# Kernel optimization log

Measured on AMD Instinct MI355X. Metric: run time of the kernel, lower is better.

The kernel has to match this reference:

```python
import jax, jax.numpy as jnp
import numpy as np

N, E, G, ND, H, C, L = 100000, 640000, 1000, 128, 128, 10, 4
ATOMS_PER_GRAPH = 100  # N = G * ATOMS_PER_GRAPH
NEG_SLOPE = 0.01  # nn.LeakyReLU default


def setup_inputs() -> dict:
    key = jax.random.key(0)
    ks = jax.random.split(key, 16)
    s = 0.05
    return {
        "node_attr": jax.random.normal(ks[0], (N, ND), jnp.float32),
        "edge_index": jax.random.randint(ks[1], (2, E), 0, N, jnp.int64),
        "num_atoms": jnp.full((G,), ATOMS_PER_GRAPH, dtype=jnp.int64),
        "enc_W": jax.random.normal(ks[2], (ND, H), jnp.float32) * s,
        "enc_b": jnp.zeros((H,), jnp.float32),
        "gcn_W": jax.random.normal(ks[3], (L, H, H), jnp.float32) * s,
        "gcn_b": jnp.zeros((L, H), jnp.float32),
        "r_W1": jax.random.normal(ks[4], (H, H), jnp.float32) * s,
        "r_b1": jnp.zeros((H,), jnp.float32),
        "r_W2": jax.random.normal(ks[5], (H, H), jnp.float32) * s,
        "r_b2": jnp.zeros((H,), jnp.float32),
        "s_W1": jax.random.normal(ks[6], (H, H), jnp.float32) * s,
        "s_b1": jnp.zeros((H,), jnp.float32),
        "s_W2": jax.random.normal(ks[7], (H, H), jnp.float32) * s,
        "s_b2": jnp.zeros((H,), jnp.float32),
        "fin_W": jax.random.normal(ks[8], (H, C), jnp.float32) * s,
        "fin_b": jnp.zeros((C,), jnp.float32),
    }


def _leaky(x):
    return jnp.where(x > 0, x, NEG_SLOPE * x)


def reference(node_attr, edge_index, num_atoms, enc_W, enc_b, gcn_W, gcn_b,
              r_W1, r_b1, r_W2, r_b2, s_W1, s_b1, s_W2, s_b2, fin_W, fin_b):
    dst, src = edge_index[0], edge_index[1]
    # degree normalization constant across layers: deg(i) = in-edge count, divide by deg+1
    deg = jax.ops.segment_sum(jnp.ones((E,), node_attr.dtype), dst, num_segments=N)
    inv_deg = 1.0 / (deg + 1.0)  # [N]

    x = node_attr @ enc_W + enc_b  # [N, H]
    for l in range(L):
        h = x @ gcn_W[l] + gcn_b[l]
        agg = jax.ops.segment_sum(h[src], dst, num_segments=N)  # scatter_sum over dst
        x = (h + agg) * inv_deg[:, None]

    # GateMLP: ReLuMLP(x) * SigmoidMLP(x)
    r = _leaky(_leaky(x @ r_W1 + r_b1) @ r_W2 + r_b2)
    g = jax.nn.sigmoid(_leaky(x @ s_W1 + s_b1) @ s_W2 + s_b2)
    x = r * g  # [N, H]

    # graph pooling: scatter_mean over graph ids
    graph_mask = jnp.repeat(jnp.arange(G), num_atoms, total_repeat_length=N)
    gsum = jax.ops.segment_sum(x, graph_mask, num_segments=G)
    cnt = jax.ops.segment_sum(jnp.ones((N,), x.dtype), graph_mask, num_segments=G)
    graph_attr = gsum / jnp.maximum(cnt, 1.0)[:, None]  # [G, H]
    return graph_attr @ fin_W + fin_b  # [G, C]
```

## Files before the change

kernel.cpp:

```cpp
#include <hip/hip_runtime.h>
#include <hip/hip_bf16.h>
#include <cstddef>
#include <cstdint>

#define CAP 32
#define LEAK 0.01f

typedef __attribute__((ext_vector_type(8))) short short8v;
typedef __attribute__((ext_vector_type(4))) float float4v;

__device__ __forceinline__ unsigned short f2bf(float f) {
    uint32_t u = __float_as_uint(f);
    uint32_t r = (u + 0x7FFFu + ((u >> 16) & 1u)) >> 16;
    return (unsigned short)r;
}
__device__ __forceinline__ float bf2f(unsigned short s) {
    return __uint_as_float(((uint32_t)s) << 16);
}

__device__ __forceinline__ void load_wf(const unsigned short* __restrict__ Wpack,
                                        int w, int fr, int fg, short8v wf[2][4]) {
    const short8v* Wp = (const short8v*)Wpack;
#pragma unroll
    for (int t = 0; t < 2; ++t)
#pragma unroll
        for (int kc = 0; kc < 4; ++kc)
            wf[t][kc] = Wp[(kc * 4 + fg) * 128 + w * 32 + t * 16 + fr];
}

__device__ __forceinline__ void load_wf_f32(const float* __restrict__ W,
                                            int w, int fr, int fg, short8v wf[2][4]) {
#pragma unroll
    for (int t = 0; t < 2; ++t) {
        const int n = w * 32 + t * 16 + fr;
#pragma unroll
        for (int kc = 0; kc < 4; ++kc) {
            short8v v;
#pragma unroll
            for (int j = 0; j < 8; ++j)
                v[j] = (short)f2bf(W[(size_t)(kc * 32 + fg * 8 + j) * 128 + n]);
            wf[t][kc] = v;
        }
    }
}

__device__ __forceinline__ void mfma_tile(const unsigned short* As, int fr, int fg,
                                          const short8v wf[2][4], float4v acc[4][2]) {
#pragma unroll
    for (int m = 0; m < 4; ++m) {
        acc[m][0] = (float4v){0.f, 0.f, 0.f, 0.f};
        acc[m][1] = (float4v){0.f, 0.f, 0.f, 0.f};
    }
#pragma unroll
    for (int kc = 0; kc < 4; ++kc) {
        short8v a[4];
#pragma unroll
        for (int m = 0; m < 4; ++m) {
            int row = m * 16 + fr;
            int cb = (kc * 64 + fg * 16) ^ ((row & 7) << 4);
            a[m] = *(const short8v*)((const char*)As + row * 256 + cb);
        }
#pragma unroll
        for (int m = 0; m < 4; ++m) {
            acc[m][0] = __builtin_amdgcn_mfma_f32_16x16x32_bf16(a[m], wf[0][kc], acc[m][0], 0, 0, 0);
            acc[m][1] = __builtin_amdgcn_mfma_f32_16x16x32_bf16(a[m], wf[1][kc], acc[m][1], 0, 0, 0);
        }
    }
}

__global__ __launch_bounds__(256) void prep(const int* __restrict__ ei, int E_,
                                            int* __restrict__ cnt,
                                            int* __restrict__ bucket,
                                            const float* __restrict__ node_attr,
                                            unsigned short* __restrict__ bx, int Nn,
                                            const float* __restrict__ enc_W,
                                            const float* __restrict__ gcn_W,
                                            const float* __restrict__ rw1,
                                            const float* __restrict__ rw2,
                                            const float* __restrict__ sw1,
                                            const float* __restrict__ sw2,
                                            const float* __restrict__ enc_b,
                                            const float* __restrict__ gcn_b,
                                            const float* __restrict__ rb1,
                                            const float* __restrict__ sb1,
                                            unsigned short* __restrict__ wpack,
                                            unsigned short* __restrict__ foldbuf,
                                            float* __restrict__ fbias,
                                            const int* __restrict__ na,
                                            int* __restrict__ goff, int G_,
                                            int NB_EDGE, int NB_CVT) {
    const int b = blockIdx.x;
    const int tid = threadIdx.x;

    if (b < NB_EDGE) {
        int e = (b * 256 + tid) * 4;
        if (e >= E_) return;
        if (e + 4 <= E_) {
            int4 d4 = *(const int4*)&ei[e];
            int4 s4 = *(const int4*)&ei[(size_t)E_ + e];
            int p0 = atomicAdd(&cnt[d4.x], 1);
            int p1 = atomicAdd(&cnt[d4.y], 1);
            int p2 = atomicAdd(&cnt[d4.z], 1);
            int p3 = atomicAdd(&cnt[d4.w], 1);
            if (p0 < CAP) bucket[(size_t)d4.x * CAP + p0] = s4.x;
            if (p1 < CAP) bucket[(size_t)d4.y * CAP + p1] = s4.y;
            if (p2 < CAP) bucket[(size_t)d4.z * CAP + p2] = s4.z;
            if (p3 < CAP) bucket[(size_t)d4.w * CAP + p3] = s4.w;
        } else {
            for (; e < E_; ++e) {
                int d = ei[e], s = ei[(size_t)E_ + e];
                int p = atomicAdd(&cnt[d], 1);
                if (p < CAP) bucket[(size_t)d * CAP + p] = s;
            }
        }
        return;
    }
    if (b < NB_EDGE + NB_CVT) {
        size_t i8 = ((size_t)(b - NB_EDGE) * 256 + tid) * 8;
        if (i8 < (size_t)Nn * 128) {
            const float* ap = node_attr + i8;
            float4v p = *(const float4v*)ap;
            float4v q = *(const float4v*)(ap + 4);
            short8v v;
            v[0] = (short)f2bf(p[0]); v[1] = (short)f2bf(p[1]);
            v[2] = (short)f2bf(p[2]); v[3] = (short)f2bf(p[3]);
            v[4] = (short)f2bf(q[0]); v[5] = (short)f2bf(q[1]);
            v[6] = (short)f2bf(q[2]); v[7] = (short)f2bf(q[3]);
            *(short8v*)(bx + i8) = v;
        }
        return;
    }
    if (b < NB_EDGE + NB_CVT + 72) {
        int pb = b - (NB_EDGE + NB_CVT);
        int m = pb >> 3;
        if (m != 6 && m != 8) return;
        int idx = (pb & 7) * 256 + tid;
        const float* W = (m == 6) ? rw2 : sw2;
        int n = idx & 127;
        int fg = (idx >> 7) & 3;
        int kc = idx >> 9;
        short8v v;
#pragma unroll
        for (int j = 0; j < 8; ++j)
            v[j] = (short)f2bf(W[(size_t)(kc * 32 + fg * 8 + j) * 128 + n]);
        *(short8v*)(wpack + (size_t)m * 16384 + (size_t)idx * 8) = v;
        return;
    }
    int fb = b - (NB_EDGE + NB_CVT + 72);
    if (fb == 0) {
        __shared__ unsigned short As[64 * 128];
        __shared__ float betaL[128];

        if (tid < 128) betaL[tid] = enc_b[tid];
        __syncthreads();
        for (int l = 0; l < 4; ++l) {
            const float* Wl = gcn_W + (size_t)l * 16384;
            float acc = 0.f;
            if (tid < 128) {
                acc = gcn_b[l * 128 + tid];
                for (int k = 0; k < 128; ++k)
                    acc = fmaf(betaL[k], Wl[(size_t)k * 128 + tid], acc);
            }
            __syncthreads();
            if (tid < 128) betaL[tid] = acc;
            __syncthreads();
        }
        if (tid < 128) {
            float a1 = rb1[tid], a2 = sb1[tid];
            for (int k = 0; k < 128; ++k) {
                float bk = betaL[k];
                a1 = fmaf(bk, rw1[(size_t)k * 128 + tid], a1);
                a2 = fmaf(bk, sw1[(size_t)k * 128 + tid], a2);
            }
            fbias[128 + tid] = a1;
            fbias[256 + tid] = a2;
        }
        __syncthreads();

        const int lane = tid & 63;
        const int w = tid >> 6;
        const int fr = lane & 15;
        const int fg = lane >> 4;
        unsigned short* f0 = foldbuf;
        unsigned short* f1 = foldbuf + 32768;
        const float* Ls[5] = {gcn_W + (size_t)3 * 16384, gcn_W + (size_t)2 * 16384,
                              gcn_W + (size_t)1 * 16384, gcn_W, enc_W};

        for (int p = 0; p < 5; ++p) {
            const unsigned short* inb = (p == 0) ? nullptr : (((p - 1) & 1) == 0 ? f0 : f1);
            unsigned short* outb = (p == 4) ? (wpack + (size_t)9 * 16384)
                                            : ((p & 1) == 0 ? f0 : f1);
            const float* Lp = Ls[p];
#pragma unroll 1
            for (int rt = 0; rt < 2; ++rt) {
                {
                    const int r = tid >> 2;
                    const int cg = tid & 3;
                    const float* Ap = Lp + (size_t)(rt * 64 + r) * 128 + cg * 32;
                    char* lbase = (char*)As + r * 256;
#pragma unroll
                    for (int i = 0; i < 4; ++i) {
                        float4v pv = *(const float4v*)(Ap + i * 8);
                        float4v qv = *(const float4v*)(Ap + i * 8 + 4);
                        short8v v;
                        v[0] = (short)f2bf(pv[0]); v[1] = (short)f2bf(pv[1]);
                        v[2] = (short)f2bf(pv[2]); v[3] = (short)f2bf(pv[3]);
                        v[4] = (short)f2bf(qv[0]); v[5] = (short)f2bf(qv[1]);
                        v[6] = (short)f2bf(qv[2]); v[7] = (short)f2bf(qv[3]);
                        int cb = (cg * 64 + i * 16) ^ ((r & 7) << 4);
                        *(short8v*)(lbase + cb) = v;
                    }
                }
                __syncthreads();

#pragma unroll 1
                for (int panel = 0; panel < 2; ++panel) {
                    short8v wf[2][4];
                    if (p == 0) load_wf_f32(panel ? sw1 : rw1, w, fr, fg, wf);
                    else        load_wf(inb + panel * 16384, w, fr, fg, wf);
                    float4v acc[4][2];
                    mfma_tile(As, fr, fg, wf, acc);
                    unsigned short* dstp = outb + panel * 16384;
#pragma unroll
                    for (int t = 0; t < 2; ++t)
#pragma unroll
                        for (int m = 0; m < 4; ++m)
#pragma unroll
                            for (int q = 0; q < 4; ++q) {
                                int r = rt * 64 + m * 16 + fg * 4 + q;
                                int c = w * 32 + t * 16 + fr;
                                dstp[(size_t)((((r >> 5) * 4 + ((r >> 3) & 3)) * 128 + c) * 8)
                                     + (r & 7)] = f2bf(acc[m][t][q]);
                            }
                }
                __syncthreads();
            }
            __threadfence();
            __syncthreads();
        }
        return;
    }
    if (fb == 1) {
        __shared__ int sh[256];
        int base = tid * 4;
        int v0 = (base + 0 < G_) ? na[base + 0] : 0;
        int v1 = (base + 1 < G_) ? na[base + 1] : 0;
        int v2 = (base + 2 < G_) ? na[base + 2] : 0;
        int v3 = (base + 3 < G_) ? na[base + 3] : 0;
        int s = v0 + v1 + v2 + v3;
        sh[tid] = s;
        __syncthreads();
        for (int ofs = 1; ofs < 256; ofs <<= 1) {
            int u = (tid >= ofs) ? sh[tid - ofs] : 0;
            __syncthreads();
            sh[tid] += u;
            __syncthreads();
        }
        int run = sh[tid] - s;
        if (tid == 0) goff[0] = 0;
        run += v0; if (base + 0 < G_) goff[base + 1] = run;
        run += v1; if (base + 1 < G_) goff[base + 2] = run;
        run += v2; if (base + 2 < G_) goff[base + 3] = run;
        run += v3; if (base + 3 < G_) goff[base + 4] = run;
    }
}

__device__ __forceinline__ void acc8(float a[8], uint4 v, float m) {
    a[0] = fmaf(m, bf2f((unsigned short)(v.x & 0xffff)), a[0]);
    a[1] = fmaf(m, bf2f((unsigned short)(v.x >> 16)), a[1]);
    a[2] = fmaf(m, bf2f((unsigned short)(v.y & 0xffff)), a[2]);
    a[3] = fmaf(m, bf2f((unsigned short)(v.y >> 16)), a[3]);
    a[4] = fmaf(m, bf2f((unsigned short)(v.z & 0xffff)), a[4]);
    a[5] = fmaf(m, bf2f((unsigned short)(v.z >> 16)), a[5]);
    a[6] = fmaf(m, bf2f((unsigned short)(v.w & 0xffff)), a[6]);
    a[7] = fmaf(m, bf2f((unsigned short)(v.w >> 16)), a[7]);
}

__device__ __forceinline__ void issue4(const char* __restrict__ xb, int2 prep_,
                                       int gl, int l16, int Nn, int jb, uint4 V[4]) {
    const int sl = gl + (jb >> 1);
    int s0 = __shfl(prep_.x, sl);
    int s1 = __shfl(prep_.y, sl);
    int s2 = __shfl(prep_.x, sl + 1);
    int s3 = __shfl(prep_.y, sl + 1);
    s0 = min(max(s0, 0), Nn - 1);
    s1 = min(max(s1, 0), Nn - 1);
    s2 = min(max(s2, 0), Nn - 1);
    s3 = min(max(s3, 0), Nn - 1);
    V[0] = *(const uint4*)(xb + (size_t)s0 * 256 + l16 * 16);
    V[1] = *(const uint4*)(xb + (size_t)s1 * 256 + l16 * 16);
    V[2] = *(const uint4*)(xb + (size_t)s2 * 256 + l16 * 16);
    V[3] = *(const uint4*)(xb + (size_t)s3 * 256 + l16 * 16);
}

__device__ __forceinline__ void consume4(float a[8], const uint4 V[4], int jb, int d) {
    acc8(a, V[0], (jb + 0 < d) ? 1.f : 0.f);
    acc8(a, V[1], (jb + 1 < d) ? 1.f : 0.f);
    acc8(a, V[2], (jb + 2 < d) ? 1.f : 0.f);
    acc8(a, V[3], (jb + 3 < d) ? 1.f : 0.f);
}

__global__ __launch_bounds__(256, 4) void agg_pass(const unsigned short* __restrict__ x,
                                                   const int* __restrict__ bucket,
                                                   const int* __restrict__ cnt,
                                                   unsigned short* __restrict__ xout,
                                                   int Nn) {
    const int tid = threadIdx.x;
    const int lane = tid & 63;
    const int w = tid >> 6;
    const int row0 = blockIdx.x * 64;
    const int l16 = lane & 15;
    const int g = lane >> 4;
    const int gl = lane & 48;
    const char* xb = (const char*)x;

    int cfull = 0;
    if (lane < 16) {
        int gn = row0 + w * 16 + lane;
        if (gn >= Nn) gn = Nn - 1;
        cfull = cnt[gn];
    }
    uint4 own[4];
    int2 pre[4];
#pragma unroll
    for (int p = 0; p < 4; ++p) {
        int gn = row0 + w * 16 + p * 4 + g;
        if (gn >= Nn) gn = Nn - 1;
        own[p] = *(const uint4*)(xb + (size_t)gn * 256 + l16 * 16);
        pre[p] = *(const int2*)&bucket[(size_t)gn * CAP + 2 * l16];
    }

#pragma unroll
    for (int p = 0; p < 4; ++p) {
        const int n = p * 4 + g;
        const int r = w * 16 + n;
        const int dfull = __shfl(cfull, n);
        const float id = 1.0f / (float)(dfull + 1);
        const int d = min(dfull, CAP);

        uint4 VA[4], VB[4];
        issue4(xb, pre[p], gl, l16, Nn, 0, VA);

        float a[8];
        {
            uint4 o = own[p];
            a[0] = bf2f((unsigned short)(o.x & 0xffff));
            a[1] = bf2f((unsigned short)(o.x >> 16));
            a[2] = bf2f((unsigned short)(o.y & 0xffff));
            a[3] = bf2f((unsigned short)(o.y >> 16));
            a[4] = bf2f((unsigned short)(o.z & 0xffff));
            a[5] = bf2f((unsigned short)(o.z >> 16));
            a[6] = bf2f((unsigned short)(o.w & 0xffff));
            a[7] = bf2f((unsigned short)(o.w >> 16));
        }

        int j = 0;
        while (true) {
            if (j + 4 < d) issue4(xb, pre[p], gl, l16, Nn, j + 4, VB);
            consume4(a, VA, j, d);
            j += 4;
            if (j >= d) break;
            if (j + 4 < d) issue4(xb, pre[p], gl, l16, Nn, j + 4, VA);
            consume4(a, VB, j, d);
            j += 4;
            if (j >= d) break;
        }

#pragma unroll
        for (int i = 0; i < 8; ++i) a[i] *= id;
        uint4 o;
        o.x = (uint32_t)f2bf(a[0]) | ((uint32_t)f2bf(a[1]) << 16);
        o.y = (uint32_t)f2bf(a[2]) | ((uint32_t)f2bf(a[3]) << 16);
        o.z = (uint32_t)f2bf(a[4]) | ((uint32_t)f2bf(a[5]) << 16);
        o.w = (uint32_t)f2bf(a[6]) | ((uint32_t)f2bf(a[7]) << 16);
        int node = row0 + r;
        if (node < Nn)
            *(uint4*)((char*)xout + (size_t)node * 256 + l16 * 16) = o;
    }
}

__global__ __launch_bounds__(512, 4) void gate_fused(const unsigned short* __restrict__ x,
                                                     const unsigned short* __restrict__ wpack,
                                                     const float* __restrict__ rb1f,
                                                     const float* __restrict__ rb2,
                                                     const float* __restrict__ sb1f,
                                                     const float* __restrict__ sb2,
                                                     unsigned short* __restrict__ out, int M) {
    __shared__ unsigned short Ws[2 * 128 * 128];
    const int tid = threadIdx.x;
    const int lane = tid & 63;
    const int w = tid >> 6;
    const int l16 = lane & 15;
    const int fg = lane >> 4;
    const int row0 = blockIdx.x * 128 + w * 16;

    int xr = row0 + l16;
    if (xr >= M) xr = M - 1;
    short8v xbf[4];
#pragma unroll
    for (int kc = 0; kc < 4; ++kc)
        xbf[kc] = *(const short8v*)(x + (size_t)xr * 128 + kc * 32 + fg * 8);

    const short8v* WL = (const short8v*)Ws;
    uint32_t upR[8][2], upS[8][2];

    union { uint32_t u[4]; short8v v; } cvt;

#define STAGE2(mi0, mi1)                                                      \
    {                                                                         \
        const short8v* s0 = (const short8v*)(wpack + (size_t)(mi0) * 16384);  \
        const short8v* s1 = (const short8v*)(wpack + (size_t)(mi1) * 16384);  \
        short8v* dst = (short8v*)Ws;                                          \
        _Pragma("unroll") for (int i = 0; i < 4; ++i)                         \
            dst[i * 512 + tid] = s0[i * 512 + tid];                          \
        _Pragma("unroll") for (int i = 0; i < 4; ++i)                         \
            dst[2048 + i * 512 + tid] = s1[i * 512 + tid];                    \
    }

#define PASS1(OFS, BIAS, UP)                                                  \
    _Pragma("unroll") for (int nt = 0; nt < 8; ++nt) {                        \
        float4v acc = (float4v){0.f, 0.f, 0.f, 0.f};                          \
        _Pragma("unroll") for (int kc = 0; kc < 4; ++kc)                      \
            acc = __builtin_amdgcn_mfma_f32_16x16x32_bf16(                    \
                WL[(OFS) + (kc * 4 + fg) * 128 + nt * 16 + l16], xbf[kc], acc, 0, 0, 0); \
        _Pragma("unroll") for (int q = 0; q < 4; ++q) {                       \
            float v = acc[q] + (BIAS)[nt * 16 + fg * 4 + q];                  \
            acc[q] = v > 0.f ? v : LEAK * v;                                  \
        }                                                                     \
        UP[nt][0] = (uint32_t)f2bf(acc[0]) | ((uint32_t)f2bf(acc[1]) << 16);  \
        UP[nt][1] = (uint32_t)f2bf(acc[2]) | ((uint32_t)f2bf(acc[3]) << 16);  \
    }

#define MKUF(UP, UF)                                                          \
    _Pragma("unroll") for (int kc = 0; kc < 4; ++kc) {                        \
        uint32_t pr0, pr1, pr2, pr3;                                          \
        {                                                                     \
            int srcl = (((2 * fg + 0) & 3) << 4) + l16;                       \
            uint32_t lo = __shfl((int)UP[2 * kc][0], srcl);                   \
            uint32_t hi = __shfl((int)UP[2 * kc + 1][0], srcl);               \
            pr0 = (fg & 2) ? hi : lo;                                         \
            lo = __shfl((int)UP[2 * kc][1], srcl);                            \
            hi = __shfl((int)UP[2 * kc + 1][1], srcl);                        \
            pr1 = (fg & 2) ? hi : lo;                                         \
        }                                                                     \
        {                                                                     \
            int srcl = (((2 * fg + 1) & 3) << 4) + l16;                       \
            uint32_t lo = __shfl((int)UP[2 * kc][0], srcl);                   \
            uint32_t hi = __shfl((int)UP[2 * kc + 1][0], srcl);               \
            pr2 = (fg & 2) ? hi : lo;                                         \
            lo = __shfl((int)UP[2 * kc][1], srcl);                            \
            hi = __shfl((int)UP[2 * kc + 1][1], srcl);                        \
            pr3 = (fg & 2) ? hi : lo;                                         \
        }                                                                     \
        cvt.u[0] = pr0; cvt.u[1] = pr1; cvt.u[2] = pr2; cvt.u[3] = pr3;       \
        UF[kc] = cvt.v;                                                       \
    }

    STAGE2(9, 10);
    __syncthreads();
    PASS1(0, rb1f, upR);
    PASS1(2048, sb1f, upS);
    __syncthreads();

    STAGE2(6, 8);
    __syncthreads();

    short8v uf[4];
    MKUF(upR, uf);
    float4v rf[8];
#pragma unroll
    for (int t2 = 0; t2 < 8; ++t2) {
        float4v acc = (float4v){0.f, 0.f, 0.f, 0.f};
#pragma unroll
        for (int kc = 0; kc < 4; ++kc)
            acc = __builtin_amdgcn_mfma_f32_16x16x32_bf16(
                uf[kc], WL[(kc * 4 + fg) * 128 + t2 * 16 + l16], acc, 0, 0, 0);
        const float bv = rb2[t2 * 16 + l16];
#pragma unroll
        for (int q = 0; q < 4; ++q) {
            float v = acc[q] + bv;
            rf[t2][q] = v > 0.f ? v : LEAK * v;
        }
    }

    MKUF(upS, uf);
#pragma unroll
    for (int t2 = 0; t2 < 8; ++t2) {
        float4v acc = (float4v){0.f, 0.f, 0.f, 0.f};
#pragma unroll
        for (int kc = 0; kc < 4; ++kc)
            acc = __builtin_amdgcn_mfma_f32_16x16x32_bf16(
                uf[kc], WL[2048 + (kc * 4 + fg) * 128 + t2 * 16 + l16], acc, 0, 0, 0);
        const float bv = sb2[t2 * 16 + l16];
#pragma unroll
        for (int q = 0; q < 4; ++q) {
            int row = row0 + fg * 4 + q;
            if (row < M) {
                float gg = 1.f / (1.f + __expf(-(acc[q] + bv)));
                out[(size_t)row * 128 + t2 * 16 + l16] = f2bf(gg * rf[t2][q]);
            }
        }
    }
#undef STAGE2
#undef PASS1
#undef MKUF
}

__global__ void pool(const unsigned short* __restrict__ x, const int* __restrict__ goff,
                     float* __restrict__ gattr, int G_) {
    int g = blockIdx.x * 2 + (threadIdx.x >> 7);
    if (g >= G_) return;
    int d = threadIdx.x & 127;
    int a0 = goff[g], a1 = goff[g + 1];
    float s0 = 0.f, s1 = 0.f, s2 = 0.f, s3 = 0.f;
    int a = a0;
    for (; a + 4 <= a1; a += 4) {
        s0 += bf2f(__builtin_nontemporal_load(&x[(size_t)(a + 0) * 128 + d]));
        s1 += bf2f(__builtin_nontemporal_load(&x[(size_t)(a + 1) * 128 + d]));
        s2 += bf2f(__builtin_nontemporal_load(&x[(size_t)(a + 2) * 128 + d]));
        s3 += bf2f(__builtin_nontemporal_load(&x[(size_t)(a + 3) * 128 + d]));
    }
    for (; a < a1; ++a) s0 += bf2f(__builtin_nontemporal_load(&x[(size_t)a * 128 + d]));
    float s = (s0 + s1) + (s2 + s3);
    float c = (float)max(a1 - a0, 1);
    gattr[(size_t)g * 128 + d] = s / c;
}

__global__ void final_gemm(const float* __restrict__ gattr, const float* __restrict__ fW,
                           const float* __restrict__ fb, float* __restrict__ out,
                           int G_, int C_) {
    int i = blockIdx.x * 256 + threadIdx.x;
    if (i >= G_ * C_) return;
    int g = i / C_, c = i % C_;
    const float* row = gattr + (size_t)g * 128;
    float s = fb[c];
    for (int k = 0; k < 128; ++k) s = fmaf(row[k], fW[k * C_ + c], s);
    out[i] = s;
}

extern "C" void kernel_launch(void* const* d_in, const int* in_sizes, int n_in,
                              void* d_out, int out_size, void* d_ws, size_t ws_size,
                              hipStream_t stream) {
    const float* node_attr = (const float*)d_in[0];
    const int* edge_index  = (const int*)d_in[1];
    const int* num_atoms   = (const int*)d_in[2];
    const float* enc_W = (const float*)d_in[3];
    const float* enc_b = (const float*)d_in[4];
    const float* gcn_W = (const float*)d_in[5];
    const float* gcn_b = (const float*)d_in[6];
    const float* r_W1 = (const float*)d_in[7];
    const float* r_b1 = (const float*)d_in[8];
    const float* r_W2 = (const float*)d_in[9];
    const float* r_b2 = (const float*)d_in[10];
    const float* s_W1 = (const float*)d_in[11];
    const float* s_b1 = (const float*)d_in[12];
    const float* s_W2 = (const float*)d_in[13];
    const float* s_b2 = (const float*)d_in[14];
    const float* fin_W = (const float*)d_in[15];
    const float* fin_b = (const float*)d_in[16];
    float* out = (float*)d_out;

    const int N_ = in_sizes[0] / 128;
    const int E_ = in_sizes[1] / 2;
    const int G_ = in_sizes[2];
    const int C_ = in_sizes[16];

    size_t off = 0;
    auto alloc = [&](size_t bytes) -> void* {
        void* p = (char*)d_ws + off;
        off += (bytes + 255) & ~(size_t)255;
        return p;
    };
    unsigned short* bx = (unsigned short*)alloc((size_t)N_ * 128 * 2);
    unsigned short* bh = (unsigned short*)alloc((size_t)N_ * 128 * 2);
    int* bucket = (int*)alloc((size_t)N_ * CAP * 4);
    int* cnt    = (int*)alloc((size_t)N_ * 4);
    unsigned short* wpack = (unsigned short*)alloc((size_t)11 * 16384 * 2);
    unsigned short* foldbuf = (unsigned short*)alloc((size_t)2 * 32768 * 2);
    float* fbias = (float*)alloc((size_t)3 * 128 * 4);
    int* goff   = (int*)alloc((size_t)(G_ + 1) * 4);
    float* gattr = (float*)alloc((size_t)G_ * 128 * 4);
    (void)ws_size; (void)n_in; (void)out_size;

    const int agg_grid = (N_ + 63) / 64;
    const int NB_EDGE = (E_ / 4 + 255) / 256;
    const int NB_CVT = (N_ * 16 + 255) / 256;
    const int NB_PREP = NB_EDGE + NB_CVT + 72 + 2;

    hipMemsetAsync(cnt, 0, (size_t)N_ * 4, stream);
    prep<<<NB_PREP, 256, 0, stream>>>(edge_index, E_, cnt, bucket,
                                      node_attr, bx, N_,
                                      enc_W, gcn_W, r_W1, r_W2, s_W1, s_W2,
                                      enc_b, gcn_b, r_b1, s_b1,
                                      wpack, foldbuf, fbias, num_atoms, goff, G_,
                                      NB_EDGE, NB_CVT);

    agg_pass<<<agg_grid, 256, 0, stream>>>(bx, bucket, cnt, bh, N_);
    agg_pass<<<agg_grid, 256, 0, stream>>>(bh, bucket, cnt, bx, N_);
    agg_pass<<<agg_grid, 256, 0, stream>>>(bx, bucket, cnt, bh, N_);
    agg_pass<<<agg_grid, 256, 0, stream>>>(bh, bucket, cnt, bx, N_);

    gate_fused<<<(N_ + 127) / 128, 512, 0, stream>>>(bx, wpack, fbias + 128, r_b2,
                                                     fbias + 256, s_b2, bh, N_);

    pool<<<(G_ + 1) / 2, 256, 0, stream>>>(bh, goff, gattr, G_);
    final_gemm<<<(G_ * C_ + 255) / 256, 256, 0, stream>>>(gattr, fin_W, fin_b, out, G_, C_);
}
```

Before: 293.7 us.

## Parallelize weight-chain folding across blocks and overlap with aggregation passes

Before, a single block folded the chain of encoder, GCN and gate first-layer weights serially with MFMA. Now the fold is split into independent 128x128 fp32 matmuls. Four of them run across 256 prep blocks, and the remaining two stages run as extra blocks appended to the first two aggregation launches. This is meant to remove the long serial tail that one block added to the prep kernel. The trade-offs are extra blocks in the agg passes and fp32 scalar FMA in place of bf16 MFMA, which also changes numerics slightly.

```diff
diff --git a/kernel.cpp b/kernel.cpp
--- a/kernel.cpp
+++ b/kernel.cpp
@@ -16,56 +16,6 @@
 }
 __device__ __forceinline__ float bf2f(unsigned short s) {
     return __uint_as_float(((uint32_t)s) << 16);
-}
-
-__device__ __forceinline__ void load_wf(const unsigned short* __restrict__ Wpack,
-                                        int w, int fr, int fg, short8v wf[2][4]) {
-    const short8v* Wp = (const short8v*)Wpack;
-#pragma unroll
-    for (int t = 0; t < 2; ++t)
-#pragma unroll
-        for (int kc = 0; kc < 4; ++kc)
-            wf[t][kc] = Wp[(kc * 4 + fg) * 128 + w * 32 + t * 16 + fr];
-}
-
-__device__ __forceinline__ void load_wf_f32(const float* __restrict__ W,
-                                            int w, int fr, int fg, short8v wf[2][4]) {
-#pragma unroll
-    for (int t = 0; t < 2; ++t) {
-        const int n = w * 32 + t * 16 + fr;
-#pragma unroll
-        for (int kc = 0; kc < 4; ++kc) {
-            short8v v;
-#pragma unroll
-            for (int j = 0; j < 8; ++j)
-                v[j] = (short)f2bf(W[(size_t)(kc * 32 + fg * 8 + j) * 128 + n]);
-            wf[t][kc] = v;
-        }
-    }
-}
-
-__device__ __forceinline__ void mfma_tile(const unsigned short* As, int fr, int fg,
-                                          const short8v wf[2][4], float4v acc[4][2]) {
-#pragma unroll
-    for (int m = 0; m < 4; ++m) {
-        acc[m][0] = (float4v){0.f, 0.f, 0.f, 0.f};
-        acc[m][1] = (float4v){0.f, 0.f, 0.f, 0.f};
-    }
-#pragma unroll
-    for (int kc = 0; kc < 4; ++kc) {
-        short8v a[4];
-#pragma unroll
-        for (int m = 0; m < 4; ++m) {
-            int row = m * 16 + fr;
-            int cb = (kc * 64 + fg * 16) ^ ((row & 7) << 4);
-            a[m] = *(const short8v*)((const char*)As + row * 256 + cb);
-        }
-#pragma unroll
-        for (int m = 0; m < 4; ++m) {
-            acc[m][0] = __builtin_amdgcn_mfma_f32_16x16x32_bf16(a[m], wf[0][kc], acc[m][0], 0, 0, 0);
-            acc[m][1] = __builtin_amdgcn_mfma_f32_16x16x32_bf16(a[m], wf[1][kc], acc[m][1], 0, 0, 0);
-        }
-    }
 }
 
 __global__ __launch_bounds__(256) void prep(const int* __restrict__ ei, int E_,
@@ -84,7 +34,7 @@
                                             const float* __restrict__ rb1,
                                             const float* __restrict__ sb1,
                                             unsigned short* __restrict__ wpack,
-                                            unsigned short* __restrict__ foldbuf,
+                                            float* __restrict__ fold32,
                                             float* __restrict__ fbias,
                                             const int* __restrict__ na,
                                             int* __restrict__ goff, int G_,
@@ -130,10 +80,9 @@
         }
         return;
     }
-    if (b < NB_EDGE + NB_CVT + 72) {
+    if (b < NB_EDGE + NB_CVT + 16) {
         int pb = b - (NB_EDGE + NB_CVT);
-        int m = pb >> 3;
-        if (m != 6 && m != 8) return;
+        int m = (pb < 8) ? 6 : 8;
         int idx = (pb & 7) * 256 + tid;
         const float* W = (m == 6) ? rw2 : sw2;
         int n = idx & 127;
@@ -146,11 +95,29 @@
         *(short8v*)(wpack + (size_t)m * 16384 + (size_t)idx * 8) = v;
         return;
     }
-    int fb = b - (NB_EDGE + NB_CVT + 72);
+    int fb = b - (NB_EDGE + NB_CVT + 16);
+    if (fb < 256) {
+        int which = fb >> 6;
+        int r = (fb & 63) * 2 + (tid >> 7);
+        int n = tid & 127;
+        const float* L;
+        const float* R;
+        switch (which) {
+            case 0: L = enc_W;                       R = gcn_W;                 break;
+            case 1: L = gcn_W + (size_t)1 * 16384;   R = gcn_W + (size_t)2 * 16384; break;
+            case 2: L = gcn_W + (size_t)3 * 16384;   R = rw1;                   break;
+            default: L = gcn_W + (size_t)3 * 16384;  R = sw1;                   break;
+        }
+        float acc = 0.f;
+#pragma unroll 8
+        for (int k = 0; k < 128; ++k)
+            acc = fmaf(L[(size_t)r * 128 + k], R[(size_t)k * 128 + n], acc);
+        fold32[(size_t)which * 16384 + (size_t)r * 128 + n] = acc;
+        return;
+    }
+    fb -= 256;
     if (fb == 0) {
-        __shared__ unsigned short As[64 * 128];
         __shared__ float betaL[128];
-
         if (tid < 128) betaL[tid] = enc_b[tid];
         __syncthreads();
         for (int l = 0; l < 4; ++l) {
@@ -174,69 +141,6 @@
             }
             fbias[128 + tid] = a1;
             fbias[256 + tid] = a2;
-        }
-        __syncthreads();
-
-        const int lane = tid & 63;
-        const int w = tid >> 6;
-        const int fr = lane & 15;
-        const int fg = lane >> 4;
-        unsigned short* f0 = foldbuf;
-        unsigned short* f1 = foldbuf + 32768;
-        const float* Ls[5] = {gcn_W + (size_t)3 * 16384, gcn_W + (size_t)2 * 16384,
-                              gcn_W + (size_t)1 * 16384, gcn_W, enc_W};
-
-        for (int p = 0; p < 5; ++p) {
-            const unsigned short* inb = (p == 0) ? nullptr : (((p - 1) & 1) == 0 ? f0 : f1);
-            unsigned short* outb = (p == 4) ? (wpack + (size_t)9 * 16384)
-                                            : ((p & 1) == 0 ? f0 : f1);
-            const float* Lp = Ls[p];
-#pragma unroll 1
-            for (int rt = 0; rt < 2; ++rt) {
-                {
-                    const int r = tid >> 2;
-                    const int cg = tid & 3;
-                    const float* Ap = Lp + (size_t)(rt * 64 + r) * 128 + cg * 32;
-                    char* lbase = (char*)As + r * 256;
-#pragma unroll
-                    for (int i = 0; i < 4; ++i) {
-                        float4v pv = *(const float4v*)(Ap + i * 8);
-                        float4v qv = *(const float4v*)(Ap + i * 8 + 4);
-                        short8v v;
-                        v[0] = (short)f2bf(pv[0]); v[1] = (short)f2bf(pv[1]);
-                        v[2] = (short)f2bf(pv[2]); v[3] = (short)f2bf(pv[3]);
-                        v[4] = (short)f2bf(qv[0]); v[5] = (short)f2bf(qv[1]);
-                        v[6] = (short)f2bf(qv[2]); v[7] = (short)f2bf(qv[3]);
-                        int cb = (cg * 64 + i * 16) ^ ((r & 7) << 4);
-                        *(short8v*)(lbase + cb) = v;
-                    }
-                }
-                __syncthreads();
-
-#pragma unroll 1
-                for (int panel = 0; panel < 2; ++panel) {
-                    short8v wf[2][4];
-                    if (p == 0) load_wf_f32(panel ? sw1 : rw1, w, fr, fg, wf);
-                    else        load_wf(inb + panel * 16384, w, fr, fg, wf);
-                    float4v acc[4][2];
-                    mfma_tile(As, fr, fg, wf, acc);
-                    unsigned short* dstp = outb + panel * 16384;
-#pragma unroll
-                    for (int t = 0; t < 2; ++t)
-#pragma unroll
-                        for (int m = 0; m < 4; ++m)
-#pragma unroll
-                            for (int q = 0; q < 4; ++q) {
-                                int r = rt * 64 + m * 16 + fg * 4 + q;
-                                int c = w * 32 + t * 16 + fr;
-                                dstp[(size_t)((((r >> 5) * 4 + ((r >> 3) & 3)) * 128 + c) * 8)
-                                     + (r & 7)] = f2bf(acc[m][t][q]);
-                            }
-                }
-                __syncthreads();
-            }
-            __threadfence();
-            __syncthreads();
         }
         return;
     }
@@ -300,11 +204,42 @@
     acc8(a, V[3], (jb + 3 < d) ? 1.f : 0.f);
 }
 
+template <int FM>
 __global__ __launch_bounds__(256, 4) void agg_pass(const unsigned short* __restrict__ x,
                                                    const int* __restrict__ bucket,
                                                    const int* __restrict__ cnt,
                                                    unsigned short* __restrict__ xout,
-                                                   int Nn) {
+                                                   int Nn, int aggGrid,
+                                                   float* __restrict__ fold32,
+                                                   unsigned short* __restrict__ wpack) {
+    if (FM != 0 && (int)blockIdx.x >= aggGrid) {
+        const int tid = threadIdx.x;
+        const int e = blockIdx.x - aggGrid;
+        if (FM == 1) {
+            int r = e * 2 + (tid >> 7), n = tid & 127;
+            const float* A = fold32;
+            const float* B = fold32 + 16384;
+            float acc = 0.f;
+#pragma unroll 8
+            for (int k = 0; k < 128; ++k)
+                acc = fmaf(A[(size_t)r * 128 + k], B[(size_t)k * 128 + n], acc);
+            fold32[65536 + (size_t)r * 128 + n] = acc;
+        } else {
+            int panel = e >> 6;
+            int r = (e & 63) * 2 + (tid >> 7), n = tid & 127;
+            const float* Ep = fold32 + 65536;
+            const float* CD = fold32 + (size_t)(2 + panel) * 16384;
+            float acc = 0.f;
+#pragma unroll 8
+            for (int k = 0; k < 128; ++k)
+                acc = fmaf(Ep[(size_t)r * 128 + k], CD[(size_t)k * 128 + n], acc);
+            int kc = r >> 5, fg2 = (r >> 3) & 3, j = r & 7;
+            wpack[(size_t)(9 + panel) * 16384 +
+                  (size_t)(((kc * 4 + fg2) * 128 + n) * 8 + j)] = f2bf(acc);
+        }
+        return;
+    }
+
     const int tid = threadIdx.x;
     const int lane = tid & 63;
     const int w = tid >> 6;
@@ -576,7 +511,7 @@
     int* bucket = (int*)alloc((size_t)N_ * CAP * 4);
     int* cnt    = (int*)alloc((size_t)N_ * 4);
     unsigned short* wpack = (unsigned short*)alloc((size_t)11 * 16384 * 2);
-    unsigned short* foldbuf = (unsigned short*)alloc((size_t)2 * 32768 * 2);
+    float* fold32 = (float*)alloc((size_t)5 * 16384 * 4);
     float* fbias = (float*)alloc((size_t)3 * 128 * 4);
     int* goff   = (int*)alloc((size_t)(G_ + 1) * 4);
     float* gattr = (float*)alloc((size_t)G_ * 128 * 4);
@@ -585,20 +520,24 @@
     const int agg_grid = (N_ + 63) / 64;
     const int NB_EDGE = (E_ / 4 + 255) / 256;
     const int NB_CVT = (N_ * 16 + 255) / 256;
-    const int NB_PREP = NB_EDGE + NB_CVT + 72 + 2;
+    const int NB_PREP = NB_EDGE + NB_CVT + 16 + 256 + 2;
 
     hipMemsetAsync(cnt, 0, (size_t)N_ * 4, stream);
     prep<<<NB_PREP, 256, 0, stream>>>(edge_index, E_, cnt, bucket,
                                       node_attr, bx, N_,
                                       enc_W, gcn_W, r_W1, r_W2, s_W1, s_W2,
                                       enc_b, gcn_b, r_b1, s_b1,
-                                      wpack, foldbuf, fbias, num_atoms, goff, G_,
+                                      wpack, fold32, fbias, num_atoms, goff, G_,
                                       NB_EDGE, NB_CVT);
 
-    agg_pass<<<agg_grid, 256, 0, stream>>>(bx, bucket, cnt, bh, N_);
-    agg_pass<<<agg_grid, 256, 0, stream>>>(bh, bucket, cnt, bx, N_);
-    agg_pass<<<agg_grid, 256, 0, stream>>>(bx, bucket, cnt, bh, N_);
-    agg_pass<<<agg_grid, 256, 0, stream>>>(bh, bucket, cnt, bx, N_);
+    agg_pass<1><<<agg_grid + 64, 256, 0, stream>>>(bx, bucket, cnt, bh, N_,
+                                                   agg_grid, fold32, wpack);
+    agg_pass<2><<<agg_grid + 128, 256, 0, stream>>>(bh, bucket, cnt, bx, N_,
+                                                    agg_grid, fold32, wpack);
+    agg_pass<0><<<agg_grid, 256, 0, stream>>>(bx, bucket, cnt, bh, N_,
+                                              agg_grid, fold32, wpack);
+    agg_pass<0><<<agg_grid, 256, 0, stream>>>(bh, bucket, cnt, bx, N_,
+                                              agg_grid, fold32, wpack);
 
     gate_fused<<<(N_ + 127) / 128, 512, 0, stream>>>(bx, wpack, fbias + 128, r_b2,
                                                      fbias + 256, s_b2, bh, N_);
```

Measured after the change: 247.1 us. 1.19x faster.
